# Performance work log

Measured on AMD Instinct MI355X. Metric: run time of the kernel, lower is better.

The kernel has to match this reference:

```python
import jax, jax.numpy as jnp
import numpy as np

N_NODES = 100000
N_GRAPHS = 64


def gcn_conv(x, src, dst, W, b, num_nodes):
    """PyG GCNConv: add self-loops, symmetric deg normalization, aggregate at dst."""
    h = x @ W  # [N, out]
    ones_e = jnp.ones(src.shape[0], dtype=x.dtype)
    # degree includes self-loop (+1)
    deg = jax.ops.segment_sum(ones_e, dst, num_segments=num_nodes) + 1.0
    dinv = jnp.where(deg > 0, 1.0 / jnp.sqrt(deg), 0.0)  # deg>=1 always here
    norm = dinv[src] * dinv[dst]  # [E]
    msg = h[src] * norm[:, None]  # gather + scale
    agg = jax.ops.segment_sum(msg, dst, num_segments=num_nodes)
    # self-loop contribution: norm_ii = dinv[i]^2
    agg = agg + h * (dinv * dinv)[:, None]
    return agg + b


def global_mean_pool(x, batch, num_graphs):
    sums = jax.ops.segment_sum(x, batch, num_segments=num_graphs)
    counts = jax.ops.segment_sum(jnp.ones(x.shape[0], dtype=x.dtype), batch,
                                 num_segments=num_graphs)
    return sums / jnp.maximum(counts, 1.0)[:, None]


def setup_inputs() -> dict:
    key = jax.random.key(0)
    ks = jax.random.split(key, 8)
    H = 128
    x = jax.random.normal(ks[0], (N_NODES, 4), dtype=jnp.float32)
    edge_index = jax.random.randint(ks[1], (2, 1600000), 0, N_NODES, dtype=jnp.int64 if jax.config.read('jax_enable_x64') else jnp.int32)
    batch = jnp.sort(jax.random.randint(ks[2], (N_NODES,), 0, N_GRAPHS))
    def glorot(k, shape):
        fan_in, fan_out = shape
        lim = np.sqrt(6.0 / (fan_in + fan_out))
        return jax.random.uniform(k, shape, jnp.float32, -lim, lim)
    return {
        'x': x,
        'edge_index': edge_index,
        'batch': batch,
        'W1': glorot(ks[3], (4, H)), 'b1': jnp.zeros((H,), jnp.float32),
        'W2': glorot(ks[4], (H, H)), 'b2': jnp.zeros((H,), jnp.float32),
        'W3': glorot(ks[5], (H, H)), 'b3': jnp.zeros((H,), jnp.float32),
        'Wl': glorot(ks[6], (H, 2)), 'bl': jnp.zeros((2,), jnp.float32),
    }


def reference(x, edge_index, batch, W1, b1, W2, b2, W3, b3, Wl, bl):
    src, dst = edge_index[0], edge_index[1]
    h = jax.nn.relu(gcn_conv(x, src, dst, W1, b1, N_NODES))
    h = jax.nn.relu(gcn_conv(h, src, dst, W2, b2, N_NODES))
    h = jax.nn.relu(gcn_conv(h, src, dst, W3, b3, N_NODES))
    g = global_mean_pool(h, batch, N_GRAPHS)  # [G, H]
    logits = g @ Wl + bl  # [G, 2]
    return jax.nn.log_softmax(logits, axis=1)
```

## Files before the change

### kernel.cpp

```cpp
#include <hip/hip_runtime.h>

#define HDIM 128
#define NGRAPH 64

#define BSHIFT 9
#define NBUCK 196
#define BCAP 48
#define BSTR 49
#define RCAP 9216
#define BIN_CHUNK 4096

typedef __attribute__((ext_vector_type(8))) short short8;
typedef __attribute__((ext_vector_type(4))) float floatx4;
typedef __attribute__((ext_vector_type(2))) float floatx2;
typedef __attribute__((ext_vector_type(4))) unsigned int uintx4;

__device__ __forceinline__ float bf2f(unsigned short u) {
    union { unsigned int i; float f; } v;
    v.i = ((unsigned int)u) << 16;
    return v.f;
}
__device__ __forceinline__ unsigned short f2bf(float f) {
    unsigned int u = __float_as_uint(f);
    u += 0x7FFFu + ((u >> 16) & 1u);
    return (unsigned short)(u >> 16);
}


__global__ __launch_bounds__(256) void k_misc(int* __restrict__ gcur,
                                              const int* __restrict__ batch,
                                              float* __restrict__ gcnt,
                                              float* __restrict__ gsum,
                                              const float* __restrict__ W2,
                                              unsigned short* __restrict__ Wp2,
                                              const float* __restrict__ W3,
                                              unsigned short* __restrict__ Wp3,
                                              int N, int nbuck) {
    int t = threadIdx.x;
    int blk = blockIdx.x;
    if (blk == 0) {
        if (t < nbuck) gcur[t] = t * RCAP;
        for (int i = t; i < NGRAPH * 128; i += 256) gsum[i] = 0.f;
        if (t < NGRAPH) {
            int g = t;
            int lo = 0, hi = N;
            while (lo < hi) { int m = (lo + hi) >> 1; if (batch[m] < g) lo = m + 1; else hi = m; }
            int lb = lo;
            lo = 0; hi = N;
            while (lo < hi) { int m = (lo + hi) >> 1; if (batch[m] < g + 1) lo = m + 1; else hi = m; }
            gcnt[g] = (float)(lo - lb);
        }
        return;
    }
    const float* W = (blk <= 64) ? W2 : W3;
    unsigned short* Wp = (blk <= 64) ? Wp2 : Wp3;
    int idx = ((blk <= 64) ? (blk - 1) : (blk - 65)) * 256 + t;
    int j = idx & 7, l = (idx >> 3) & 63, frag = idx >> 9;
    int c = frag >> 2, ks = frag & 3;
    int k = ks * 32 + ((l >> 4) & 3) * 8 + j;
    int n = c * 16 + (l & 15);
    Wp[idx] = f2bf(W[k * 128 + n]);
}


__global__ __launch_bounds__(256) void k_binA(const int* __restrict__ src,
                                              const int* __restrict__ dst,
                                              int* __restrict__ gcur,
                                              unsigned int* __restrict__ binned, int E) {
    __shared__ unsigned int bin[NBUCK * BSTR];
    __shared__ int bcnt[NBUCK];
    __shared__ int bbase[NBUCK];
    int t = threadIdx.x;
    for (int b = t; b < NBUCK; b += 256) bcnt[b] = 0;
    __syncthreads();
    int e0 = blockIdx.x * BIN_CHUNK;
    #pragma unroll
    for (int i = 0; i < BIN_CHUNK / 1024; i++) {
        int e = e0 + i * 1024 + t * 4;
        if (e + 3 < E) {
            const int4 d4 = *(const int4*)&dst[e];
            const int4 s4 = *(const int4*)&src[e];
            int dd[4] = {d4.x, d4.y, d4.z, d4.w};
            int ss[4] = {s4.x, s4.y, s4.z, s4.w};
            #pragma unroll
            for (int k = 0; k < 4; k++) {
                int d = dd[k];
                unsigned int rec = ((unsigned int)(d & 511) << 20) | (unsigned int)ss[k];
                int b = d >> BSHIFT;
                int idx = atomicAdd(&bcnt[b], 1);
                if (idx < BCAP) bin[b * BSTR + idx] = rec;
                else { int p = atomicAdd(&gcur[b], 1); binned[p] = rec; }
            }
        } else {
            for (int k = 0; k < 4; k++) {
                int e2 = e + k;
                if (e2 < E) {
                    int d = dst[e2];
                    unsigned int rec = ((unsigned int)(d & 511) << 20) | (unsigned int)src[e2];
                    int b = d >> BSHIFT;
                    int idx = atomicAdd(&bcnt[b], 1);
                    if (idx < BCAP) bin[b * BSTR + idx] = rec;
                    else { int p = atomicAdd(&gcur[b], 1); binned[p] = rec; }
                }
            }
        }
    }
    __syncthreads();
    if (t < NBUCK) {
        int cnt = min(bcnt[t], BCAP);
        bbase[t] = atomicAdd(&gcur[t], cnt);
    }
    __syncthreads();
    int wave = t >> 6, lane = t & 63;
    for (int b = wave; b < NBUCK; b += 4) {
        int cnt = min(bcnt[b], BCAP);
        int base = bbase[b];
        if (lane < cnt) binned[base + lane] = bin[b * BSTR + lane];
    }
}

__global__ __launch_bounds__(256) void k_fillB(const int* __restrict__ gcur,
                                               const unsigned int* __restrict__ binned,
                                               int* __restrict__ P,
                                               float* __restrict__ dinv,
                                               int* __restrict__ csr,
                                               const float4* __restrict__ x4,
                                               float4* __restrict__ xs4,
                                               int N, int nbuck) {
    __shared__ int ps[256];
    __shared__ int cnt[512];
    __shared__ int image[RCAP];
    int b = blockIdx.x;
    int t = threadIdx.x;
    int lt = (t < nbuck) ? (gcur[t] - t * RCAP) : 0;
    ps[t] = lt;
    __syncthreads();
    for (int d = 1; d < 256; d <<= 1) {
        int o = (t >= d) ? ps[t - d] : 0;
        __syncthreads();
        ps[t] += o;
        __syncthreads();
    }
    int start = (b > 0) ? ps[b - 1] : 0;
    int len = ps[b] - start;
    __syncthreads();

    int n0 = b << BSHIFT;
    int nloc = min(n0 + 512, N) - n0;
    cnt[t] = 0; cnt[t + 256] = 0;
    __syncthreads();
    const unsigned int* rb = binned + (size_t)b * RCAP;
    for (int i = t; i < len; i += 256) atomicAdd(&cnt[rb[i] >> 20], 1);
    __syncthreads();
    int c0 = cnt[2 * t], c1 = cnt[2 * t + 1];
    int pair = c0 + c1;
    __syncthreads();
    cnt[t] = pair;
    __syncthreads();
    for (int d = 1; d < 256; d <<= 1) {
        int o = (t >= d) ? cnt[t - d] : 0;
        __syncthreads();
        cnt[t] += o;
        __syncthreads();
    }
    int excl = cnt[t] - pair;
    __syncthreads();
    if (2 * t < nloc) {
        int n = n0 + 2 * t;
        float dv0 = rsqrtf((float)c0 + 1.0f);
        P[n] = start + excl;
        dinv[n] = dv0;
        float4 xv = x4[n];
        xs4[n] = make_float4(xv.x * dv0, xv.y * dv0, xv.z * dv0, xv.w * dv0);
    }
    if (2 * t + 1 < nloc) {
        int n = n0 + 2 * t + 1;
        float dv1 = rsqrtf((float)c1 + 1.0f);
        P[n] = start + excl + c0;
        dinv[n] = dv1;
        float4 xv = x4[n];
        xs4[n] = make_float4(xv.x * dv1, xv.y * dv1, xv.z * dv1, xv.w * dv1);
    }
    if (b == nbuck - 1 && t == 0) P[N] = start + len;
    cnt[2 * t] = excl;
    cnt[2 * t + 1] = excl + c0;
    __syncthreads();
    for (int i = t; i < len; i += 256) {
        unsigned int rec = rb[i];
        int pos = atomicAdd(&cnt[rec >> 20], 1);
        image[pos] = (int)(rec & 0xFFFFFu);
    }
    __syncthreads();
    for (int i = t; i < len; i += 256) csr[start + i] = image[i];
}

__global__ void k_aggx4(const int* __restrict__ P, const int* __restrict__ csr,
                        const float4* __restrict__ xs, const float* __restrict__ dinv,
                        float4* __restrict__ aggx, int N) {
    int idx = blockIdx.x * blockDim.x + threadIdx.x;
    int d = idx >> 2, l = idx & 3;
    if (d >= N) return;
    int s0 = P[d], s1 = P[d + 1];
    float ax = 0.f, ay = 0.f, az = 0.f, aw = 0.f;
    int i = s0 + l;
    for (; i + 4 < s1; i += 8) {
        int e0 = csr[i], e1 = csr[i + 4];
        float4 v0 = xs[e0], v1 = xs[e1];
        ax += v0.x + v1.x; ay += v0.y + v1.y;
        az += v0.z + v1.z; aw += v0.w + v1.w;
    }
    if (i < s1) {
        float4 v = xs[csr[i]];
        ax += v.x; ay += v.y; az += v.z; aw += v.w;
    }
    ax += __shfl_xor(ax, 1); ay += __shfl_xor(ay, 1);
    az += __shfl_xor(az, 1); aw += __shfl_xor(aw, 1);
    ax += __shfl_xor(ax, 2); ay += __shfl_xor(ay, 2);
    az += __shfl_xor(az, 2); aw += __shfl_xor(aw, 2);
    if (l == 0) {
        float dd = dinv[d];
        float4 sv = xs[d];
        aggx[d] = make_float4((ax + sv.x * dd) * dd, (ay + sv.y * dd) * dd,
                              (az + sv.z * dd) * dd, (aw + sv.w * dd) * dd);
    }
}

#define LXS 136
#define LFPS 144
__global__ __launch_bounds__(256) void k_l1t2(const float4* __restrict__ aggx,
                                              const float* __restrict__ W1,
                                              const float* __restrict__ b1,
                                              const unsigned short* __restrict__ Wp,
                                              const float* __restrict__ dinv,
                                              unsigned char* __restrict__ out8, int N) {
    __shared__ unsigned short lx[64 * LXS];
    __shared__ unsigned short lw[16384];
    __shared__ float w1s[512];
    __shared__ float b1s[128];
    __shared__ float ax[64][4];
    int t = threadIdx.x;
    int n0 = blockIdx.x * 64;

    for (int i = t; i < 512; i += 256) w1s[i] = W1[i];
    if (t < 128) b1s[t] = b1[t];
    if (t < 64) {
        float4 v = (n0 + t < N) ? aggx[n0 + t] : make_float4(0.f, 0.f, 0.f, 0.f);
        ax[t][0] = v.x; ax[t][1] = v.y; ax[t][2] = v.z; ax[t][3] = v.w;
    }
    for (int ch = t; ch < 2048; ch += 256)
        *(uint4*)&lw[ch * 8] = *(const uint4*)&Wp[ch * 8];
    __syncthreads();

    for (int i = t; i < 8192; i += 256) {
        int n = i >> 7, j = i & 127;
        float v = b1s[j] + ax[n][0] * w1s[j] + ax[n][1] * w1s[128 + j]
                         + ax[n][2] * w1s[256 + j] + ax[n][3] * w1s[384 + j];
        lx[n * LXS + j] = f2bf(fmaxf(v, 0.f));
    }
    __syncthreads();

    int w = t >> 6, lane = t & 63;
    int m0 = w * 16;
    int col = lane & 15, quad = lane >> 4;

    short8 afrag[4];
    #pragma unroll
    for (int ks = 0; ks < 4; ks++)
        afrag[ks] = *(const short8*)&lx[(m0 + col) * LXS + ks * 32 + quad * 8];

    float dv[4];
    #pragma unroll
    for (int r = 0; r < 4; r++) {
        int gn = n0 + m0 + quad * 4 + r;
        dv[r] = (gn < N) ? dinv[gn] : 0.0f;
    }
    __syncthreads();
    unsigned char* lfp = (unsigned char*)lx;

    #pragma unroll
    for (int c = 0; c < 8; c++) {
        floatx4 acc = {0.f, 0.f, 0.f, 0.f};
        #pragma unroll
        for (int ks = 0; ks < 4; ks++) {
            const short8 bfrag = *(const short8*)&lw[((c * 4 + ks) * 64 + lane) * 8];
            acc = __builtin_amdgcn_mfma_f32_16x16x32_bf16(afrag[ks], bfrag, acc, 0, 0, 0);
        }
        int j = c * 16 + col;
        #pragma unroll
        for (int r = 0; r < 4; r++) {
            int nl = m0 + quad * 4 + r;
            float v = acc[r] * dv[r];
            lfp[nl * LFPS + j] =
                (unsigned char)(__builtin_amdgcn_cvt_pk_fp8_f32(v, v, 0, false) & 0xFF);
        }
    }
    __syncthreads();
    #pragma unroll
    for (int k = 0; k < 2; k++) {
        int ch = t + k * 256;
        int s = ch >> 7;
        int idx2 = ch & 127;
        int nl = idx2 >> 1;
        int k0 = (idx2 & 1) * 16;
        int gn = n0 + nl;
        if (gn < N)
            *(uintx4*)&out8[(size_t)s * N * 32 + (size_t)gn * 32 + k0] =
                *(const uintx4*)&lfp[nl * LFPS + s * 32 + k0];
    }
}

__global__ __launch_bounds__(256) void k_transform_mfma(const unsigned short* __restrict__ in,
                                                        const unsigned short* __restrict__ Wp,
                                                        const float* __restrict__ dinv,
                                                        unsigned char* __restrict__ out8, int N) {
    __shared__ unsigned short lx[64 * LXS];
    __shared__ unsigned short lw[16384];
    int t = threadIdx.x;
    int n0 = blockIdx.x * 64;

    for (int ch = t; ch < 1024; ch += 256) {
        int row = ch >> 4, part = ch & 15;
        uint4 val = make_uint4(0, 0, 0, 0);
        if (n0 + row < N) val = *(const uint4*)&in[(size_t)(n0 + row) * 128 + part * 8];
        *(uint4*)&lx[row * LXS + part * 8] = val;
    }
    for (int ch = t; ch < 2048; ch += 256)
        *(uint4*)&lw[ch * 8] = *(const uint4*)&Wp[ch * 8];
    __syncthreads();

    int w = t >> 6, lane = t & 63;
    int m0 = w * 16;
    int col = lane & 15, quad = lane >> 4;

    short8 afrag[4];
    #pragma unroll
    for (int ks = 0; ks < 4; ks++)
        afrag[ks] = *(const short8*)&lx[(m0 + col) * LXS + ks * 32 + quad * 8];

    float dv[4];
    #pragma unroll
    for (int r = 0; r < 4; r++) {
        int gn = n0 + m0 + quad * 4 + r;
        dv[r] = (gn < N) ? dinv[gn] : 0.0f;
    }
    __syncthreads();
    unsigned char* lfp = (unsigned char*)lx;

    #pragma unroll
    for (int c = 0; c < 8; c++) {
        floatx4 acc = {0.f, 0.f, 0.f, 0.f};
        #pragma unroll
        for (int ks = 0; ks < 4; ks++) {
            const short8 bfrag = *(const short8*)&lw[((c * 4 + ks) * 64 + lane) * 8];
            acc = __builtin_amdgcn_mfma_f32_16x16x32_bf16(afrag[ks], bfrag, acc, 0, 0, 0);
        }
        int j = c * 16 + col;
        #pragma unroll
        for (int r = 0; r < 4; r++) {
            int nl = m0 + quad * 4 + r;
            float v = acc[r] * dv[r];
            lfp[nl * LFPS + j] =
                (unsigned char)(__builtin_amdgcn_cvt_pk_fp8_f32(v, v, 0, false) & 0xFF);
        }
    }
    __syncthreads();
    #pragma unroll
    for (int k = 0; k < 2; k++) {
        int ch = t + k * 256;
        int s = ch >> 7;
        int idx2 = ch & 127;
        int nl = idx2 >> 1;
        int k0 = (idx2 & 1) * 16;
        int gn = n0 + nl;
        if (gn < N)
            *(uintx4*)&out8[(size_t)s * N * 32 + (size_t)gn * 32 + k0] =
                *(const uintx4*)&lfp[nl * LFPS + s * 32 + k0];
    }
}

__device__ __forceinline__ void dec8x2(uint4 u, floatx2* a) {
    a[0] += __builtin_amdgcn_cvt_pk_f32_fp8(u.x, false);
    a[1] += __builtin_amdgcn_cvt_pk_f32_fp8(u.x, true);
    a[2] += __builtin_amdgcn_cvt_pk_f32_fp8(u.y, false);
    a[3] += __builtin_amdgcn_cvt_pk_f32_fp8(u.y, true);
    a[4] += __builtin_amdgcn_cvt_pk_f32_fp8(u.z, false);
    a[5] += __builtin_amdgcn_cvt_pk_f32_fp8(u.z, true);
    a[6] += __builtin_amdgcn_cvt_pk_f32_fp8(u.w, false);
    a[7] += __builtin_amdgcn_cvt_pk_f32_fp8(u.w, true);
}

__global__ __launch_bounds__(256) void k_agg_sl(const int* __restrict__ P,
                                                const int* __restrict__ csr,
                                                const unsigned int* __restrict__ tab,
                                                const float* __restrict__ dinv,
                                                const float* __restrict__ bias,
                                                unsigned short* __restrict__ out16,
                                                const int* __restrict__ batch,
                                                float* __restrict__ gsum,
                                                int N, int mode) {
    __shared__ float psum[32][32];
    int t = threadIdx.x;
    int bid = blockIdx.x;
    int xcd = bid & 7;
    int slice = xcd >> 1;
    int chunk = (bid >> 3) * 2 + (xcd & 1);
    int nb = chunk * 32;
    int grp = t >> 3;
    int lg = t & 7;
    int slot = lg >> 1;
    int half = lg & 1;
    int g = nb + grp;
    const unsigned int* sl = tab + (size_t)slice * N * 8;
    int hofs = half * 4;

    floatx2 a2[8];
    #pragma unroll
    for (int j = 0; j < 8; j++) a2[j] = (floatx2){0.f, 0.f};

    if (g < N) {
        int s0 = P[g], s1 = P[g + 1];
        int i = s0;
        for (; i + 8 <= s1; i += 8) {
            int e0 = csr[i + slot];
            int e1 = csr[i + slot + 4];
            uint4 u0 = *(const uint4*)&sl[(size_t)e0 * 8 + hofs];
            uint4 u1 = *(const uint4*)&sl[(size_t)e1 * 8 + hofs];
            dec8x2(u0, a2);
            dec8x2(u1, a2);
        }
        if (i + 4 <= s1) {
            int e = csr[i + slot];
            uint4 u = *(const uint4*)&sl[(size_t)e * 8 + hofs];
            dec8x2(u, a2);
            i += 4;
        }
        int k = i + slot;
        if (k < s1) {
            int e = csr[k];
            uint4 u = *(const uint4*)&sl[(size_t)e * 8 + hofs];
            dec8x2(u, a2);
        }
        if (slot == 0) {
            uint4 su = *(const uint4*)&sl[(size_t)g * 8 + hofs];
            dec8x2(su, a2);
        }
    }

    #pragma unroll
    for (int j = 0; j < 8; j++) {
        union { double d; floatx2 f; } u, v;
        u.f = a2[j];
        v.d = __shfl_xor(u.d, 2);
        a2[j] += v.f;
        u.f = a2[j];
        v.d = __shfl_xor(u.d, 4);
        a2[j] += v.f;
    }

    float o[16];
    #pragma unroll
    for (int j = 0; j < 16; j++) o[j] = 0.f;
    if (g < N) {
        float dd = dinv[g];
        const float* bb = &bias[slice * 32 + half * 16];
        #pragma unroll
        for (int j = 0; j < 16; j++) {
            float av = a2[j >> 1][j & 1];
            o[j] = fmaxf(av * dd + bb[j], 0.f);
        }
        if (mode == 0 && slot == 0) {
            uintx4 w0, w1;
            w0.x = (unsigned int)f2bf(o[0]) | ((unsigned int)f2bf(o[1]) << 16);
            w0.y = (unsigned int)f2bf(o[2]) | ((unsigned int)f2bf(o[3]) << 16);
            w0.z = (unsigned int)f2bf(o[4]) | ((unsigned int)f2bf(o[5]) << 16);
            w0.w = (unsigned int)f2bf(o[6]) | ((unsigned int)f2bf(o[7]) << 16);
            w1.x = (unsigned int)f2bf(o[8]) | ((unsigned int)f2bf(o[9]) << 16);
            w1.y = (unsigned int)f2bf(o[10]) | ((unsigned int)f2bf(o[11]) << 16);
            w1.z = (unsigned int)f2bf(o[12]) | ((unsigned int)f2bf(o[13]) << 16);
            w1.w = (unsigned int)f2bf(o[14]) | ((unsigned int)f2bf(o[15]) << 16);
            unsigned short* dst = &out16[(size_t)g * 128 + slice * 32 + half * 16];
            __builtin_nontemporal_store(w0, (uintx4*)dst);
            __builtin_nontemporal_store(w1, (uintx4*)(dst + 8));
        }
    }
    if (mode != 0) {
        if (slot == 0) {
            #pragma unroll
            for (int q = 0; q < 4; q++)
                *(float4*)&psum[grp][half * 16 + q * 4] =
                    make_float4(o[q * 4], o[q * 4 + 1], o[q * 4 + 2], o[q * 4 + 3]);
        }
        __syncthreads();
        if (t < 32 && nb < N) {
            int f = t;
            int nbN = min(32, N - nb);
            int b0 = batch[nb], bL = batch[nb + nbN - 1];
            if (b0 == bL) {
                float s = 0.f;
                #pragma unroll
                for (int n = 0; n < 32; n++) s += psum[n][f];
                unsafeAtomicAdd(&gsum[(size_t)b0 * 128 + slice * 32 + f], s);
            } else {
                float acc = 0.f; int cur = b0;
                for (int n = 0; n < nbN; n++) {
                    int bb = batch[nb + n];
                    if (bb != cur) {
                        unsafeAtomicAdd(&gsum[(size_t)cur * 128 + slice * 32 + f], acc);
                        acc = 0.f; cur = bb;
                    }
                    acc += psum[n][f];
                }
                unsafeAtomicAdd(&gsum[(size_t)cur * 128 + slice * 32 + f], acc);
            }
        }
    }
}

__global__ __launch_bounds__(256) void k_head(const float* __restrict__ gsum,
                                              const float* __restrict__ gcnt,
                                              const float* __restrict__ Wl,
                                              const float* __restrict__ bl,
                                              float* __restrict__ out, int G) {
    int t = threadIdx.x;
    int g = t >> 2, q = t & 3;
    if (g >= G) return;
    float l0 = 0.f, l1 = 0.f;
    #pragma unroll
    for (int k = 0; k < 32; k++) {
        int jj = q * 32 + k;
        float v = gsum[(size_t)g * 128 + jj];
        l0 += v * Wl[jj * 2 + 0];
        l1 += v * Wl[jj * 2 + 1];
    }
    l0 += __shfl_xor(l0, 1, 64); l1 += __shfl_xor(l1, 1, 64);
    l0 += __shfl_xor(l0, 2, 64); l1 += __shfl_xor(l1, 2, 64);
    if (q == 0) {
        float inv = 1.0f / fmaxf(gcnt[g], 1.0f);
        l0 = l0 * inv + bl[0];
        l1 = l1 * inv + bl[1];
        float m = fmaxf(l0, l1);
        float lse = m + logf(expf(l0 - m) + expf(l1 - m));
        out[g * 2 + 0] = l0 - lse;
        out[g * 2 + 1] = l1 - lse;
    }
}


extern "C" void kernel_launch(void* const* d_in, const int* in_sizes, int n_in,
                              void* d_out, int out_size, void* d_ws, size_t ws_size,
                              hipStream_t stream) {
    const float* x   = (const float*)d_in[0];
    const int*   ei  = (const int*)d_in[1];
    const int*   bat = (const int*)d_in[2];
    const float* W1  = (const float*)d_in[3];
    const float* b1  = (const float*)d_in[4];
    const float* W2  = (const float*)d_in[5];
    const float* b2  = (const float*)d_in[6];
    const float* W3  = (const float*)d_in[7];
    const float* b3  = (const float*)d_in[8];
    const float* Wl  = (const float*)d_in[9];
    const float* bl  = (const float*)d_in[10];

    const int N = in_sizes[0] / 4;
    const int E = in_sizes[1] / 2;
    const int* srcI = ei;
    const int* dstI = ei + E;

    const int nbuck = (N + 511) >> BSHIFT;
    const int pAlloc = ((N + 1 + 3) & ~3) + 4;

    float* wsf  = (float*)d_ws;
    float* dinv = wsf;
    int*   P    = (int*)(dinv + N);
    int*   csr  = P + pAlloc;
    float* aggx = (float*)(csr + E);
    unsigned short* bufA16 = (unsigned short*)(aggx + (size_t)N * 4);
    unsigned char*  hs8    = (unsigned char*)(bufA16 + (size_t)N * 128);
    unsigned short* Wp2    = (unsigned short*)(hs8 + (size_t)N * 128);
    unsigned short* Wp3    = Wp2 + 16384;
    float* gsum = (float*)(Wp3 + 16384);
    float* gcnt = gsum + NGRAPH * 128;
    int*   gcur = (int*)(gcnt + NGRAPH);
    unsigned int* binned = (unsigned int*)hs8;
    float* xs4 = (float*)bufA16;

    const int chunks = (N + 31) >> 5;
    const int aggGrid = ((chunks + 1) >> 1) * 8;

    k_misc<<<129, 256, 0, stream>>>(gcur, bat, gcnt, gsum, W2, Wp2, W3, Wp3, N, nbuck);
    k_binA<<<(E + BIN_CHUNK - 1) / BIN_CHUNK, 256, 0, stream>>>(srcI, dstI, gcur, binned, E);
    k_fillB<<<nbuck, 256, 0, stream>>>(gcur, binned, P, dinv, csr,
                                       (const float4*)x, (float4*)xs4, N, nbuck);

    k_aggx4<<<(N * 4 + 255) / 256, 256, 0, stream>>>(P, csr, (const float4*)xs4, dinv,
                                                     (float4*)aggx, N);
    k_l1t2<<<(N + 63) / 64, 256, 0, stream>>>((const float4*)aggx, W1, b1, Wp2, dinv, hs8, N);

    k_agg_sl<<<aggGrid, 256, 0, stream>>>(P, csr, (const unsigned int*)hs8,
                                          dinv, b2, bufA16, nullptr, nullptr, N, 0);

    k_transform_mfma<<<(N + 63) / 64, 256, 0, stream>>>(bufA16, Wp3, dinv, hs8, N);
    k_agg_sl<<<aggGrid, 256, 0, stream>>>(P, csr, (const unsigned int*)hs8,
                                          dinv, b3, nullptr, bat, gsum, N, 1);

    k_head<<<1, 256, 0, stream>>>(gsum, gcnt, Wl, bl, (float*)d_out, NGRAPH);
}
```

Measured before the change: 278.9 us.

## Fuse layer-1 aggregation into transform kernel and enlarge binning chunks

The standalone 4-wide aggregation kernel is removed. Its per-node gather and reduction now runs inside the layer-1 transform kernel, with 64 nodes per block and 4 threads per node, writing straight to shared memory. This removes one launch and the write and read back of the aggx intermediate. The binning kernel also processes twice as many edges per block, with larger per-bucket LDS bins and a strided flush loop. That reduces global atomic overflow, but the larger LDS use may lower occupancy.

```diff
diff --git a/kernel.cpp b/kernel.cpp
--- a/kernel.cpp
+++ b/kernel.cpp
@@ -5,10 +5,10 @@
 
 #define BSHIFT 9
 #define NBUCK 196
-#define BCAP 48
-#define BSTR 49
+#define BCAP 84
+#define BSTR 85
 #define RCAP 9216
-#define BIN_CHUNK 4096
+#define BIN_CHUNK 8192
 
 typedef __attribute__((ext_vector_type(8))) short short8;
 typedef __attribute__((ext_vector_type(4))) float floatx4;
@@ -115,7 +115,7 @@
     for (int b = wave; b < NBUCK; b += 4) {
         int cnt = min(bcnt[b], BCAP);
         int base = bbase[b];
-        if (lane < cnt) binned[base + lane] = bin[b * BSTR + lane];
+        for (int j = lane; j < cnt; j += 64) binned[base + j] = bin[b * BSTR + j];
     }
 }
 
@@ -194,40 +194,11 @@
     for (int i = t; i < len; i += 256) csr[start + i] = image[i];
 }
 
-__global__ void k_aggx4(const int* __restrict__ P, const int* __restrict__ csr,
-                        const float4* __restrict__ xs, const float* __restrict__ dinv,
-                        float4* __restrict__ aggx, int N) {
-    int idx = blockIdx.x * blockDim.x + threadIdx.x;
-    int d = idx >> 2, l = idx & 3;
-    if (d >= N) return;
-    int s0 = P[d], s1 = P[d + 1];
-    float ax = 0.f, ay = 0.f, az = 0.f, aw = 0.f;
-    int i = s0 + l;
-    for (; i + 4 < s1; i += 8) {
-        int e0 = csr[i], e1 = csr[i + 4];
-        float4 v0 = xs[e0], v1 = xs[e1];
-        ax += v0.x + v1.x; ay += v0.y + v1.y;
-        az += v0.z + v1.z; aw += v0.w + v1.w;
-    }
-    if (i < s1) {
-        float4 v = xs[csr[i]];
-        ax += v.x; ay += v.y; az += v.z; aw += v.w;
-    }
-    ax += __shfl_xor(ax, 1); ay += __shfl_xor(ay, 1);
-    az += __shfl_xor(az, 1); aw += __shfl_xor(aw, 1);
-    ax += __shfl_xor(ax, 2); ay += __shfl_xor(ay, 2);
-    az += __shfl_xor(az, 2); aw += __shfl_xor(aw, 2);
-    if (l == 0) {
-        float dd = dinv[d];
-        float4 sv = xs[d];
-        aggx[d] = make_float4((ax + sv.x * dd) * dd, (ay + sv.y * dd) * dd,
-                              (az + sv.z * dd) * dd, (aw + sv.w * dd) * dd);
-    }
-}
-
 #define LXS 136
 #define LFPS 144
-__global__ __launch_bounds__(256) void k_l1t2(const float4* __restrict__ aggx,
+__global__ __launch_bounds__(256) void k_l1t2(const int* __restrict__ P,
+                                              const int* __restrict__ csr,
+                                              const float4* __restrict__ xs,
                                               const float* __restrict__ W1,
                                               const float* __restrict__ b1,
                                               const unsigned short* __restrict__ Wp,
@@ -243,12 +214,44 @@
 
     for (int i = t; i < 512; i += 256) w1s[i] = W1[i];
     if (t < 128) b1s[t] = b1[t];
-    if (t < 64) {
-        float4 v = (n0 + t < N) ? aggx[n0 + t] : make_float4(0.f, 0.f, 0.f, 0.f);
-        ax[t][0] = v.x; ax[t][1] = v.y; ax[t][2] = v.z; ax[t][3] = v.w;
-    }
     for (int ch = t; ch < 2048; ch += 256)
         *(uint4*)&lw[ch * 8] = *(const uint4*)&Wp[ch * 8];
+
+    {
+        int d = n0 + (t >> 2), l = t & 3;
+        float axx = 0.f, ayy = 0.f, azz = 0.f, aww = 0.f;
+        if (d < N) {
+            int s0 = P[d], s1 = P[d + 1];
+            int i = s0 + l;
+            for (; i + 4 < s1; i += 8) {
+                int e0 = csr[i], e1 = csr[i + 4];
+                float4 v0 = xs[e0], v1 = xs[e1];
+                axx += v0.x + v1.x; ayy += v0.y + v1.y;
+                azz += v0.z + v1.z; aww += v0.w + v1.w;
+            }
+            if (i < s1) {
+                float4 v = xs[csr[i]];
+                axx += v.x; ayy += v.y; azz += v.z; aww += v.w;
+            }
+        }
+        axx += __shfl_xor(axx, 1); ayy += __shfl_xor(ayy, 1);
+        azz += __shfl_xor(azz, 1); aww += __shfl_xor(aww, 1);
+        axx += __shfl_xor(axx, 2); ayy += __shfl_xor(ayy, 2);
+        azz += __shfl_xor(azz, 2); aww += __shfl_xor(aww, 2);
+        if (l == 0) {
+            int nl = t >> 2;
+            if (d < N) {
+                float dd = dinv[d];
+                float4 sv = xs[d];
+                ax[nl][0] = (axx + sv.x * dd) * dd;
+                ax[nl][1] = (ayy + sv.y * dd) * dd;
+                ax[nl][2] = (azz + sv.z * dd) * dd;
+                ax[nl][3] = (aww + sv.w * dd) * dd;
+            } else {
+                ax[nl][0] = 0.f; ax[nl][1] = 0.f; ax[nl][2] = 0.f; ax[nl][3] = 0.f;
+            }
+        }
+    }
     __syncthreads();
 
     for (int i = t; i < 8192; i += 256) {
@@ -592,9 +595,8 @@
     k_fillB<<<nbuck, 256, 0, stream>>>(gcur, binned, P, dinv, csr,
                                        (const float4*)x, (float4*)xs4, N, nbuck);
 
-    k_aggx4<<<(N * 4 + 255) / 256, 256, 0, stream>>>(P, csr, (const float4*)xs4, dinv,
-                                                     (float4*)aggx, N);
-    k_l1t2<<<(N + 63) / 64, 256, 0, stream>>>((const float4*)aggx, W1, b1, Wp2, dinv, hs8, N);
+    k_l1t2<<<(N + 63) / 64, 256, 0, stream>>>(P, csr, (const float4*)xs4, W1, b1,
+                                              Wp2, dinv, hs8, N);
 
     k_agg_sl<<<aggGrid, 256, 0, stream>>>(P, csr, (const unsigned int*)hs8,
                                           dinv, b2, bufA16, nullptr, nullptr, N, 0);
```

Measured after the change: 275.3 us. No clear change (-1.3%).
